# Performance work log

Hardware: AMD Instinct MI355X
Metric: run time of the kernel (lower is better)

Reference implementation:

```python
import jax, jax.numpy as jnp
import numpy as np

B, C, H, W = 2, 256, 64, 64
NUM_HEADS = 4
DIM_HEAD_QK = 64
DIM_HEAD_V = 64  # dim_out // num_heads
DIM_OUT_QK = NUM_HEADS * DIM_HEAD_QK  # 256
DIM_OUT_V = NUM_HEADS * DIM_HEAD_V    # 256
SCALE = DIM_HEAD_QK ** -0.5


def rel_logits_1d(q, rel_k, permute):
    # q: (Bh, Hq, Wq, d), rel_k: (2*Wq-1, d)
    Bh, Hq, Wq, d = q.shape
    R = 2 * Wq - 1
    x = jnp.einsum('bhwd,rd->bhwr', q, rel_k)              # (Bh, Hq, Wq, R)
    x = x.reshape(-1, Wq, R)
    x_pad = jnp.pad(x, ((0, 0), (0, 0), (0, 1))).reshape(x.shape[0], -1)
    x_pad = jnp.pad(x_pad, ((0, 0), (0, Wq - 1)))
    x_pad = x_pad.reshape(-1, Wq + 1, R)
    x = x_pad[:, :Wq, Wq - 1:]                              # (Bh*Hq, Wq, Wq)
    x = x.reshape(Bh, Hq, 1, Wq, Wq)
    x = jnp.broadcast_to(x, (Bh, Hq, Hq, Wq, Wq))
    return jnp.transpose(x, permute)


def pos_embed_rel(q, height_rel, width_rel):
    # q: (Bh, HW, d)
    Bh = q.shape[0]
    qr = q.reshape(Bh, H, W, -1)
    rel_w = rel_logits_1d(qr, width_rel, (0, 1, 3, 2, 4))   # (Bh, H, W, H, W)
    qt = jnp.transpose(qr, (0, 2, 1, 3))                    # (Bh, W, H, d)
    rel_h = rel_logits_1d(qt, height_rel, (0, 3, 1, 4, 2))  # (Bh, H, W, H, W)
    return (rel_h + rel_w).reshape(Bh, H * W, H * W)


def setup_inputs() -> dict:
    key = jax.random.key(0)
    k1, k2, k3, k4 = jax.random.split(key, 4)
    x = jax.random.normal(k1, (B, C, H, W), dtype=jnp.float32)
    qkv_w = jax.random.normal(k2, (2 * DIM_OUT_QK + DIM_OUT_V, C), dtype=jnp.float32) * (C ** -0.5)
    height_rel = jax.random.normal(k3, (2 * H - 1, DIM_HEAD_QK), dtype=jnp.float32) * SCALE
    width_rel = jax.random.normal(k4, (2 * W - 1, DIM_HEAD_QK), dtype=jnp.float32) * SCALE
    return {"x": x, "qkv_w": qkv_w, "height_rel": height_rel, "width_rel": width_rel}


def reference(x, qkv_w, height_rel, width_rel):
    # 1x1 conv == channel matmul
    qkv = jnp.einsum('bchw,oc->bohw', x, qkv_w)             # (B, 768, H, W)
    q, k, v = jnp.split(qkv, [DIM_OUT_QK, 2 * DIM_OUT_QK], axis=1)
    HW = H * W
    q = q.reshape(B * NUM_HEADS, DIM_HEAD_QK, HW).transpose(0, 2, 1)  # (Bh, HW, d)
    k = k.reshape(B * NUM_HEADS, DIM_HEAD_QK, HW)                     # (Bh, d, HW)
    v = v.reshape(B * NUM_HEADS, DIM_HEAD_V, HW).transpose(0, 2, 1)   # (Bh, HW, dv)
    attn = jnp.einsum('bnd,bdm->bnm', q, k) * SCALE + pos_embed_rel(q, height_rel, width_rel)
    attn = jax.nn.softmax(attn, axis=-1)
    out = jnp.einsum('bnm,bmd->bnd', attn, v)               # (Bh, HW, dv)
    out = out.transpose(0, 2, 1).reshape(B, DIM_OUT_V, H, W)
    return out
```

## Files before the change

kernel.cpp:

```cpp
#include <hip/hip_runtime.h>
#include <hip/hip_bf16.h>

typedef __attribute__((ext_vector_type(8))) short bf16x8;
typedef __attribute__((ext_vector_type(4))) float f32x4;

static __device__ __forceinline__ f32x4 mfma16(bf16x8 a, bf16x8 b, f32x4 c) {
    return __builtin_amdgcn_mfma_f32_16x16x32_bf16(a, b, c, 0, 0, 0);
}
static __device__ __forceinline__ void gll16(const void* g, void* l) {
    __builtin_amdgcn_global_load_lds(
        (const __attribute__((address_space(1))) unsigned int*)g,
        (__attribute__((address_space(3))) unsigned int*)l, 16, 0, 0);
}

#define LOG2E 1.44269504f

__global__ __launch_bounds__(256, 4) void qkv_kernel(
    const float* __restrict__ x, const float* __restrict__ w,
    __hip_bfloat16* __restrict__ qb, __hip_bfloat16* __restrict__ kb,
    __hip_bfloat16* __restrict__ vt)
{
    alignas(16) __shared__ __hip_bfloat16 sA[64 * 72];
    alignas(16) __shared__ __hip_bfloat16 sB[64 * 72];
    const int nb = blockIdx.x * 64;
    const int ob = blockIdx.y * 64;
    const int b  = blockIdx.z;
    const int tid  = threadIdx.x;
    const int lane = tid & 63;
    const int wv   = tid >> 6;
    const int quad = lane >> 4;
    const int l16  = lane & 15;

    f32x4 acc[4];
    for (int i = 0; i < 4; i++) acc[i] = (f32x4)0.f;

    for (int k0 = 0; k0 < 256; k0 += 64) {
        __syncthreads();
        {
            const int o = tid >> 2, c0 = (tid & 3) << 4;
            const float* srcw = w + (ob + o) * 256 + k0 + c0;
            union { bf16x8 v; __hip_bfloat16 h[8]; } u0, u1;
            #pragma unroll
            for (int i = 0; i < 2; i++) {
                float4 f = *(const float4*)(srcw + i * 4);
                u0.h[4*i+0] = __float2bfloat16(f.x); u0.h[4*i+1] = __float2bfloat16(f.y);
                u0.h[4*i+2] = __float2bfloat16(f.z); u0.h[4*i+3] = __float2bfloat16(f.w);
            }
            #pragma unroll
            for (int i = 0; i < 2; i++) {
                float4 f = *(const float4*)(srcw + 8 + i * 4);
                u1.h[4*i+0] = __float2bfloat16(f.x); u1.h[4*i+1] = __float2bfloat16(f.y);
                u1.h[4*i+2] = __float2bfloat16(f.z); u1.h[4*i+3] = __float2bfloat16(f.w);
            }
            *(bf16x8*)&sA[o * 72 + c0]     = u0.v;
            *(bf16x8*)&sA[o * 72 + c0 + 8] = u1.v;
        }
        {
            const int c = tid >> 2, n0 = (tid & 3) << 4;
            const int csw = c ^ ((tid & 3) * 16);
            const float* srcx = x + ((size_t)b * 256 + k0 + c) * 4096 + nb + n0;
            #pragma unroll
            for (int i = 0; i < 4; i++) {
                float4 f = *(const float4*)(srcx + i * 4);
                sB[(n0 + 4*i + 0) * 72 + csw] = __float2bfloat16(f.x);
                sB[(n0 + 4*i + 1) * 72 + csw] = __float2bfloat16(f.y);
                sB[(n0 + 4*i + 2) * 72 + csw] = __float2bfloat16(f.z);
                sB[(n0 + 4*i + 3) * 72 + csw] = __float2bfloat16(f.w);
            }
        }
        __syncthreads();
        const __hip_bfloat16* aRow = &sA[(16 * wv + l16) * 72];
        #pragma unroll
        for (int ks = 0; ks < 2; ks++) {
            bf16x8 af = *(const bf16x8*)&aRow[ks * 32 + quad * 8];
            #pragma unroll
            for (int ct = 0; ct < 4; ct++) {
                bf16x8 bfv = *(const bf16x8*)&sB[(16 * ct + l16) * 72
                                                 + ((ks * 32 + quad * 8) ^ (ct * 16))];
                acc[ct] = mfma16(af, bfv, acc[ct]);
            }
        }
    }
    if (ob < 512) {
        #pragma unroll
        for (int ct = 0; ct < 4; ct++) {
            int n = nb + 16 * ct + l16;
            int o0 = ob + 16 * wv + quad * 4;
            union { short4 s; __hip_bfloat16 hh[4]; } u;
            #pragma unroll
            for (int r = 0; r < 4; r++) u.hh[r] = __float2bfloat16(acc[ct][r]);
            int oo = o0 & 255;
            int bhh = b * 4 + (oo >> 6), d = oo & 63;
            if (o0 < 256) {
                *(short4*)(qb + ((size_t)bhh * 4096 + n) * 64 + d) = u.s;
            } else {
                *(short4*)(kb + ((size_t)bhh * 4096 + n) * 64 + (d ^ ((n & 7) << 3))) = u.s;
            }
        }
    } else {
        __syncthreads();
        #pragma unroll
        for (int ct = 0; ct < 4; ct++)
            #pragma unroll
            for (int r = 0; r < 4; r++)
                sA[(16 * wv + quad * 4 + r) * 72 + 16 * ct + l16] = __float2bfloat16(acc[ct][r]);
        int o2 = (ob - 512) + 16 * wv + l16;
        int bhh = b * 4 + (o2 >> 6), d = o2 & 63;
        const __hip_bfloat16* srcl = &sA[(16 * wv + l16) * 72 + 16 * quad];
        __hip_bfloat16* vrow = vt + ((size_t)bhh * 64 + d) * 4096;
        const int kt = quad & 1;
        const int gbase = nb + (quad >> 1) * 32;
        const int dsw = (d & 7) << 3;
        #pragma unroll
        for (int m = 0; m < 4; m++) {
            short4 val = *(const short4*)(srcl + 4 * m);
            int P4 = gbase + 8 * m + 4 * kt;
            *(short4*)(vrow + (P4 ^ dsw)) = val;
        }
    }
}

__global__ __launch_bounds__(512, 4) void attn_kernel(
    const __hip_bfloat16* __restrict__ qb, const __hip_bfloat16* __restrict__ kb,
    const __hip_bfloat16* __restrict__ vt, const float* __restrict__ hrel,
    const float* __restrict__ wrel, float* __restrict__ out)
{
    extern __shared__ __align__(16) char smem[];
    alignas(16) __shared__ __hip_bfloat16 sRH[64 * 66];

    const int h    = blockIdx.x;
    const int bh   = blockIdx.y;
    const int tid  = threadIdx.x;
    const int lane = tid & 63;
    const int wv   = tid >> 6;
    const int qg   = wv >> 2;
    const int kg   = wv & 3;
    const int quad = lane >> 4;
    const int l16  = lane & 15;

    __hip_bfloat16* sQ   = (__hip_bfloat16*)smem;
    __hip_bfloat16* sW   = (__hip_bfloat16*)smem + 64 * 72;
    __hip_bfloat16* sHRs = (__hip_bfloat16*)smem + 192 * 72;
    __hip_bfloat16* sRWt = (__hip_bfloat16*)smem;

    {
        int r = tid >> 3, d8 = (tid & 7) * 8;
        *(bf16x8*)&sQ[r * 72 + d8] =
            *(const bf16x8*)&qb[(((size_t)bh * 4096 + h * 64 + r)) * 64 + d8];
    }
    {
        int r = tid >> 2, c0 = (tid & 3) << 4;
        union { bf16x8 v; __hip_bfloat16 h8[8]; } u0, u1;
        #pragma unroll
        for (int i = 0; i < 2; i++) {
            float4 f = (r < 127) ? *(const float4*)&wrel[r * 64 + c0 + 4*i] : float4{0,0,0,0};
            u0.h8[4*i+0] = __float2bfloat16(f.x); u0.h8[4*i+1] = __float2bfloat16(f.y);
            u0.h8[4*i+2] = __float2bfloat16(f.z); u0.h8[4*i+3] = __float2bfloat16(f.w);
        }
        #pragma unroll
        for (int i = 0; i < 2; i++) {
            float4 f = (r < 127) ? *(const float4*)&wrel[r * 64 + c0 + 8 + 4*i] : float4{0,0,0,0};
            u1.h8[4*i+0] = __float2bfloat16(f.x); u1.h8[4*i+1] = __float2bfloat16(f.y);
            u1.h8[4*i+2] = __float2bfloat16(f.z); u1.h8[4*i+3] = __float2bfloat16(f.w);
        }
        *(bf16x8*)&sW[r * 72 + c0]     = u0.v;
        *(bf16x8*)&sW[r * 72 + c0 + 8] = u1.v;
    }
    {
        int r = tid >> 3, c0 = (tid & 7) * 8;
        union { bf16x8 v; __hip_bfloat16 h8[8]; } u0;
        #pragma unroll
        for (int i = 0; i < 2; i++) {
            float4 f = *(const float4*)&hrel[(63 - h + r) * 64 + c0 + 4*i];
            u0.h8[4*i+0] = __float2bfloat16(f.x); u0.h8[4*i+1] = __float2bfloat16(f.y);
            u0.h8[4*i+2] = __float2bfloat16(f.z); u0.h8[4*i+3] = __float2bfloat16(f.w);
        }
        *(bf16x8*)&sHRs[r * 72 + c0] = u0.v;
    }
    __syncthreads();

    const int g    = wv & 3;
    const int half = wv >> 2;
    const __hip_bfloat16* aRow = &sQ[(16 * g + l16) * 72];
    bf16x8 qf0 = *(const bf16x8*)&aRow[quad * 8];
    bf16x8 qf1 = *(const bf16x8*)&aRow[32 + quad * 8];
    bf16x8 qm[2][2];
    #pragma unroll
    for (int qt = 0; qt < 2; qt++) {
        const __hip_bfloat16* qr = &sQ[(qg * 32 + 16 * qt + l16) * 72];
        qm[qt][0] = *(const bf16x8*)&qr[quad * 8];
        qm[qt][1] = *(const bf16x8*)&qr[32 + quad * 8];
    }
    __syncthreads();

    {
        const int rbase = half * 64;
        #pragma unroll
        for (int ct = 0; ct < 4; ct++) {
            int rr = rbase + 16 * ct + l16;
            f32x4 a = (f32x4)0.f;
            a = mfma16(qf0, *(const bf16x8*)&sW[rr * 72 + quad * 8], a);
            a = mfma16(qf1, *(const bf16x8*)&sW[rr * 72 + 32 + quad * 8], a);
            #pragma unroll
            for (int r = 0; r < 4; r++) {
                int ww = 16 * g + quad * 4 + r;
                int wp = rr + ww - 63;
                if (wp >= 0 && wp < 64) sRWt[ww * 68 + wp] = __float2bfloat16(a[r]);
            }
        }
    }
    if (half == 0) {
        #pragma unroll
        for (int ct = 0; ct < 4; ct++) {
            f32x4 a = (f32x4)0.f;
            a = mfma16(qf0, *(const bf16x8*)&sHRs[(16 * ct + l16) * 72 + quad * 8], a);
            a = mfma16(qf1, *(const bf16x8*)&sHRs[(16 * ct + l16) * 72 + 32 + quad * 8], a);
            #pragma unroll
            for (int r = 0; r < 4; r++)
                sRH[(16 * g + quad * 4 + r) * 66 + 16 * ct + l16] = __float2bfloat16(a[r]);
        }
    }
    __syncthreads();

    union S4 { short4 s; __hip_bfloat16 h[4]; };
    S4 rwp[2][2];
    #pragma unroll
    for (int qt = 0; qt < 2; qt++)
        #pragma unroll
        for (int kt = 0; kt < 2; kt++)
            rwp[qt][kt].s = *(const short4*)&sRWt[(qg * 32 + 16 * qt + l16) * 68
                                                  + 32 * (kg & 1) + 16 * kt + 4 * quad];
    __syncthreads();

    const char* kT = (const char*)kb + (size_t)bh * 524288 + wv * 1024 + lane * 16;
    const char* vT = (const char*)vt + (size_t)bh * 524288
                     + (size_t)(wv * 4 + quad) * 8192 + l16 * 16;

    gll16(kT,           smem + wv * 1024);
    gll16(kT + 8192,    smem + 8192 + wv * 1024);
    gll16(vT,           smem + 16384 + wv * 1024);
    gll16(vT + 262144,  smem + 24576 + wv * 1024);
    __syncthreads();

    f32x4 oacc[2][4];
    #pragma unroll
    for (int qt = 0; qt < 2; qt++)
        #pragma unroll
        for (int dt = 0; dt < 4; dt++) oacc[qt][dt] = (f32x4)0.f;
    float lsum[2] = {0.f, 0.f};

    const int krowOff = (kg * 32 + l16) * 128;
    const int sw  = (l16 & 7) << 4;
    const int kA  = (quad * 16) ^ sw;
    const int kB  = (64 + quad * 16) ^ sw;
    const int vOff = 16384 + l16 * 256 + ((kg * 64 + quad * 16) ^ sw);

    const __hip_bfloat16* rh0 = &sRH[(qg * 32 + l16) * 66];
    const __hip_bfloat16* rh1 = &sRH[(qg * 32 + 16 + l16) * 66];

    for (int j = 0; j < 32; j++) {
        const char* buf = smem + (j & 1) * 32768;
        if (j < 31) {
            char* nbuf = smem + ((j + 1) & 1) * 32768;
            const char* gk = kT + (size_t)(j + 1) * 16384;
            gll16(gk,          nbuf + wv * 1024);
            gll16(gk + 8192,   nbuf + 8192 + wv * 1024);
            const char* gv = vT + (size_t)(j + 1) * 256;
            gll16(gv,          nbuf + 16384 + wv * 1024);
            gll16(gv + 262144, nbuf + 24576 + wv * 1024);
        }

        const char* kr = buf + krowOff;
        bf16x8 kf00 = *(const bf16x8*)(kr + kA);
        bf16x8 kf01 = *(const bf16x8*)(kr + kB);
        bf16x8 kf10 = *(const bf16x8*)(kr + 2048 + kA);
        bf16x8 kf11 = *(const bf16x8*)(kr + 2048 + kB);

        const int hp = 2 * j + (kg >> 1);
        bf16x8 pa[2];
        #pragma unroll
        for (int qt = 0; qt < 2; qt++) {
            f32x4 s0 = (f32x4)0.f, s1 = (f32x4)0.f;
            s0 = mfma16(kf00, qm[qt][0], s0);
            s0 = mfma16(kf01, qm[qt][1], s0);
            s1 = mfma16(kf10, qm[qt][0], s1);
            s1 = mfma16(kf11, qm[qt][1], s1);
            float rhb = LOG2E * __bfloat162float((qt ? rh1 : rh0)[hp]);
            union { bf16x8 v; __hip_bfloat16 hh[8]; } pu;
            #pragma unroll
            for (int r = 0; r < 4; r++) {
                float p = __builtin_amdgcn_exp2f(
                    fmaf(s0[r], 0.125f * LOG2E,
                         fmaf(__bfloat162float(rwp[qt][0].h[r]), LOG2E, rhb)));
                lsum[qt] += p;
                pu.hh[r] = __float2bfloat16(p);
            }
            #pragma unroll
            for (int r = 0; r < 4; r++) {
                float p = __builtin_amdgcn_exp2f(
                    fmaf(s1[r], 0.125f * LOG2E,
                         fmaf(__bfloat162float(rwp[qt][1].h[r]), LOG2E, rhb)));
                lsum[qt] += p;
                pu.hh[4 + r] = __float2bfloat16(p);
            }
            pa[qt] = pu.v;
        }

        #pragma unroll
        for (int dt = 0; dt < 4; dt++) {
            bf16x8 vf = *(const bf16x8*)(buf + vOff + dt * 4096);
            oacc[0][dt] = mfma16(pa[0], vf, oacc[0][dt]);
            oacc[1][dt] = mfma16(pa[1], vf, oacc[1][dt]);
        }
        __syncthreads();
    }

    #pragma unroll
    for (int qt = 0; qt < 2; qt++) {
        lsum[qt] += __shfl_xor(lsum[qt], 16, 64);
        lsum[qt] += __shfl_xor(lsum[qt], 32, 64);
    }

    float* obuf  = (float*)smem;
    float* slbuf = obuf + 4608;
    for (int rnd = 1; rnd < 4; rnd++) {
        if (kg == rnd) {
            #pragma unroll
            for (int qt = 0; qt < 2; qt++)
                #pragma unroll
                for (int dt = 0; dt < 4; dt++)
                    *(f32x4*)&obuf[qg * 2304 + (16 * dt + l16) * 36 + 16 * qt + 4 * quad]
                        = oacc[qt][dt];
            if (quad == 0) {
                slbuf[qg * 64 + l16]      = lsum[0];
                slbuf[qg * 64 + 16 + l16] = lsum[1];
            }
        }
        __syncthreads();
        if (kg == 0) {
            #pragma unroll
            for (int qt = 0; qt < 2; qt++)
                #pragma unroll
                for (int dt = 0; dt < 4; dt++)
                    oacc[qt][dt] += *(const f32x4*)&obuf[qg * 2304 + (16 * dt + l16) * 36
                                                          + 16 * qt + 4 * quad];
            lsum[0] += slbuf[qg * 64 + l16];
            lsum[1] += slbuf[qg * 64 + 16 + l16];
        }
        __syncthreads();
    }

    if (kg == 0) {
        if (quad == 0) {
            slbuf[qg * 64 + l16]      = lsum[0];
            slbuf[qg * 64 + 16 + l16] = lsum[1];
        }
        const int b = bh >> 2, head = bh & 3;
        #pragma unroll
        for (int qt = 0; qt < 2; qt++) {
            f32x4 lv;
            #pragma unroll
            for (int r = 0; r < 4; r++)
                lv[r] = 1.f / slbuf[qg * 64 + 16 * qt + 4 * quad + r];
            #pragma unroll
            for (int dt = 0; dt < 4; dt++) {
                f32x4 o = oacc[qt][dt] * lv;
                int dv = 16 * dt + l16;
                int q0 = qg * 32 + 16 * qt + 4 * quad;
                *(f32x4*)&out[((size_t)(b * 256 + head * 64 + dv)) * 4096 + h * 64 + q0] = o;
            }
        }
    }
}

extern "C" void kernel_launch(void* const* d_in, const int* in_sizes, int n_in,
                              void* d_out, int out_size, void* d_ws, size_t ws_size,
                              hipStream_t stream) {
    const float* x     = (const float*)d_in[0];
    const float* qkv_w = (const float*)d_in[1];
    const float* hrel  = (const float*)d_in[2];
    const float* wrel  = (const float*)d_in[3];
    float* out = (float*)d_out;

    __hip_bfloat16* qb = (__hip_bfloat16*)d_ws;
    __hip_bfloat16* kb = qb + (size_t)8 * 4096 * 64;
    __hip_bfloat16* vt = kb + (size_t)8 * 4096 * 64;

    qkv_kernel<<<dim3(64, 12, 2), 256, 0, stream>>>(x, qkv_w, qb, kb, vt);
    attn_kernel<<<dim3(64, 8), 512, 65536, stream>>>(qb, kb, vt, hrel, wrel, out);
}
```

Before: 131.5 us.

## Compute softmax row sums via MFMA, stage QK stores through LDS, single-pass reduction

Several changes land together. The QKV kernel now stages Q/K tiles through shared memory so each thread writes two 16-byte vectors instead of scattered 8-byte stores. The attention loop precomputes LOG2E-scaled relative-width biases, uses paired bf16 conversion, and replaces per-lane scalar row-sum accumulation with an extra MFMA against a ones vector. It also adds s_setprio around the MFMA phases and collapses the three-round cross-warp reduction into one write and one read phase. The extra MFMAs and larger LDS reduction buffers are the trade-off for fewer VALU ops and fewer barriers.

```diff
diff --git a/kernel.cpp b/kernel.cpp
--- a/kernel.cpp
+++ b/kernel.cpp
@@ -82,20 +82,30 @@
         }
     }
     if (ob < 512) {
+        __syncthreads();
         #pragma unroll
         for (int ct = 0; ct < 4; ct++) {
-            int n = nb + 16 * ct + l16;
-            int o0 = ob + 16 * wv + quad * 4;
             union { short4 s; __hip_bfloat16 hh[4]; } u;
             #pragma unroll
             for (int r = 0; r < 4; r++) u.hh[r] = __float2bfloat16(acc[ct][r]);
-            int oo = o0 & 255;
-            int bhh = b * 4 + (oo >> 6), d = oo & 63;
-            if (o0 < 256) {
-                *(short4*)(qb + ((size_t)bhh * 4096 + n) * 64 + d) = u.s;
-            } else {
-                *(short4*)(kb + ((size_t)bhh * 4096 + n) * 64 + (d ^ ((n & 7) << 3))) = u.s;
-            }
+            *(short4*)&sA[(16 * ct + l16) * 72 + 16 * wv + 4 * quad] = u.s;
+        }
+        __syncthreads();
+        const int n_l = tid >> 2, d16 = (tid & 3) * 16;
+        const int n = nb + n_l;
+        const __hip_bfloat16* srcl = &sA[n_l * 72 + d16];
+        bf16x8 v0 = *(const bf16x8*)srcl;
+        bf16x8 v1 = *(const bf16x8*)(srcl + 8);
+        const int bhh = b * 4 + ((ob & 255) >> 6);
+        if (ob < 256) {
+            __hip_bfloat16* dst = qb + ((size_t)bhh * 4096 + n) * 64;
+            *(bf16x8*)(dst + d16)     = v0;
+            *(bf16x8*)(dst + d16 + 8) = v1;
+        } else {
+            const int s = (n & 7) << 3;
+            __hip_bfloat16* dst = kb + ((size_t)bhh * 4096 + n) * 64;
+            *(bf16x8*)(dst + (d16 ^ s))       = v0;
+            *(bf16x8*)(dst + ((d16 + 8) ^ s)) = v1;
         }
     } else {
         __syncthreads();
@@ -223,13 +233,18 @@
     __syncthreads();
 
     union S4 { short4 s; __hip_bfloat16 h[4]; };
-    S4 rwp[2][2];
+    float rwf[2][2][4];
     #pragma unroll
     for (int qt = 0; qt < 2; qt++)
         #pragma unroll
-        for (int kt = 0; kt < 2; kt++)
-            rwp[qt][kt].s = *(const short4*)&sRWt[(qg * 32 + 16 * qt + l16) * 68
-                                                  + 32 * (kg & 1) + 16 * kt + 4 * quad];
+        for (int kt = 0; kt < 2; kt++) {
+            S4 t;
+            t.s = *(const short4*)&sRWt[(qg * 32 + 16 * qt + l16) * 68
+                                        + 32 * (kg & 1) + 16 * kt + 4 * quad];
+            #pragma unroll
+            for (int r = 0; r < 4; r++)
+                rwf[qt][kt][r] = LOG2E * __bfloat162float(t.h[r]);
+        }
     __syncthreads();
 
     const char* kT = (const char*)kb + (size_t)bh * 524288 + wv * 1024 + lane * 16;
@@ -247,7 +262,8 @@
     for (int qt = 0; qt < 2; qt++)
         #pragma unroll
         for (int dt = 0; dt < 4; dt++) oacc[qt][dt] = (f32x4)0.f;
-    float lsum[2] = {0.f, 0.f};
+    f32x4 lacc[2] = {(f32x4)0.f, (f32x4)0.f};
+    const bf16x8 vones = (bf16x8)(short)0x3F80;
 
     const int krowOff = (kg * 32 + l16) * 128;
     const int sw  = (l16 & 7) << 4;
@@ -257,6 +273,7 @@
 
     const __hip_bfloat16* rh0 = &sRH[(qg * 32 + l16) * 66];
     const __hip_bfloat16* rh1 = &sRH[(qg * 32 + 16 + l16) * 66];
+    const float SC = 0.125f * LOG2E;
 
     for (int j = 0; j < 32; j++) {
         const char* buf = smem + (j & 1) * 32768;
@@ -276,92 +293,89 @@
         bf16x8 kf10 = *(const bf16x8*)(kr + 2048 + kA);
         bf16x8 kf11 = *(const bf16x8*)(kr + 2048 + kB);
 
+        f32x4 s[2][2];
+        __builtin_amdgcn_s_setprio(1);
+        #pragma unroll
+        for (int qt = 0; qt < 2; qt++) {
+            f32x4 a0 = (f32x4)0.f, a1 = (f32x4)0.f;
+            a0 = mfma16(kf00, qm[qt][0], a0);
+            a0 = mfma16(kf01, qm[qt][1], a0);
+            a1 = mfma16(kf10, qm[qt][0], a1);
+            a1 = mfma16(kf11, qm[qt][1], a1);
+            s[qt][0] = a0; s[qt][1] = a1;
+        }
+        __builtin_amdgcn_s_setprio(0);
+
         const int hp = 2 * j + (kg >> 1);
         bf16x8 pa[2];
         #pragma unroll
         for (int qt = 0; qt < 2; qt++) {
-            f32x4 s0 = (f32x4)0.f, s1 = (f32x4)0.f;
-            s0 = mfma16(kf00, qm[qt][0], s0);
-            s0 = mfma16(kf01, qm[qt][1], s0);
-            s1 = mfma16(kf10, qm[qt][0], s1);
-            s1 = mfma16(kf11, qm[qt][1], s1);
             float rhb = LOG2E * __bfloat162float((qt ? rh1 : rh0)[hp]);
-            union { bf16x8 v; __hip_bfloat16 hh[8]; } pu;
-            #pragma unroll
-            for (int r = 0; r < 4; r++) {
-                float p = __builtin_amdgcn_exp2f(
-                    fmaf(s0[r], 0.125f * LOG2E,
-                         fmaf(__bfloat162float(rwp[qt][0].h[r]), LOG2E, rhb)));
-                lsum[qt] += p;
-                pu.hh[r] = __float2bfloat16(p);
-            }
-            #pragma unroll
-            for (int r = 0; r < 4; r++) {
-                float p = __builtin_amdgcn_exp2f(
-                    fmaf(s1[r], 0.125f * LOG2E,
-                         fmaf(__bfloat162float(rwp[qt][1].h[r]), LOG2E, rhb)));
-                lsum[qt] += p;
-                pu.hh[4 + r] = __float2bfloat16(p);
-            }
+            float pv[8];
+            #pragma unroll
+            for (int r = 0; r < 4; r++)
+                pv[r] = __builtin_amdgcn_exp2f(fmaf(s[qt][0][r], SC, rwf[qt][0][r] + rhb));
+            #pragma unroll
+            for (int r = 0; r < 4; r++)
+                pv[4 + r] = __builtin_amdgcn_exp2f(fmaf(s[qt][1][r], SC, rwf[qt][1][r] + rhb));
+            union { bf16x8 v; __hip_bfloat162 b2[4]; } pu;
+            #pragma unroll
+            for (int pi = 0; pi < 4; pi++)
+                pu.b2[pi] = __float22bfloat162_rn(float2{pv[2 * pi], pv[2 * pi + 1]});
             pa[qt] = pu.v;
         }
 
+        __builtin_amdgcn_s_setprio(1);
         #pragma unroll
         for (int dt = 0; dt < 4; dt++) {
             bf16x8 vf = *(const bf16x8*)(buf + vOff + dt * 4096);
             oacc[0][dt] = mfma16(pa[0], vf, oacc[0][dt]);
             oacc[1][dt] = mfma16(pa[1], vf, oacc[1][dt]);
         }
-        __syncthreads();
-    }
-
-    #pragma unroll
-    for (int qt = 0; qt < 2; qt++) {
-        lsum[qt] += __shfl_xor(lsum[qt], 16, 64);
-        lsum[qt] += __shfl_xor(lsum[qt], 32, 64);
-    }
-
-    float* obuf  = (float*)smem;
-    float* slbuf = obuf + 4608;
-    for (int rnd = 1; rnd < 4; rnd++) {
-        if (kg == rnd) {
+        lacc[0] = mfma16(pa[0], vones, lacc[0]);
+        lacc[1] = mfma16(pa[1], vones, lacc[1]);
+        __builtin_amdgcn_s_setprio(0);
+        __syncthreads();
+    }
+
+    float* obuf = (float*)smem;
+    if (kg != 0) {
+        float* rb = obuf + (kg - 1) * 4672;
+        #pragma unroll
+        for (int qt = 0; qt < 2; qt++)
+            #pragma unroll
+            for (int dt = 0; dt < 4; dt++)
+                *(f32x4*)&rb[qg * 2304 + (16 * dt + l16) * 36 + 16 * qt + 4 * quad]
+                    = oacc[qt][dt];
+        if (l16 == 0)
             #pragma unroll
             for (int qt = 0; qt < 2; qt++)
                 #pragma unroll
-                for (int dt = 0; dt < 4; dt++)
-                    *(f32x4*)&obuf[qg * 2304 + (16 * dt + l16) * 36 + 16 * qt + 4 * quad]
-                        = oacc[qt][dt];
-            if (quad == 0) {
-                slbuf[qg * 64 + l16]      = lsum[0];
-                slbuf[qg * 64 + 16 + l16] = lsum[1];
-            }
-        }
-        __syncthreads();
-        if (kg == 0) {
-            #pragma unroll
-            for (int qt = 0; qt < 2; qt++)
+                for (int r = 0; r < 4; r++)
+                    rb[4608 + qg * 32 + 16 * qt + 4 * quad + r] = lacc[qt][r];
+    }
+    __syncthreads();
+    if (kg == 0) {
+        #pragma unroll
+        for (int rg = 0; rg < 3; rg++) {
+            const float* rb = obuf + rg * 4672;
+            #pragma unroll
+            for (int qt = 0; qt < 2; qt++) {
                 #pragma unroll
                 for (int dt = 0; dt < 4; dt++)
-                    oacc[qt][dt] += *(const f32x4*)&obuf[qg * 2304 + (16 * dt + l16) * 36
-                                                          + 16 * qt + 4 * quad];
-            lsum[0] += slbuf[qg * 64 + l16];
-            lsum[1] += slbuf[qg * 64 + 16 + l16];
-        }
-        __syncthreads();
-    }
-
-    if (kg == 0) {
-        if (quad == 0) {
-            slbuf[qg * 64 + l16]      = lsum[0];
-            slbuf[qg * 64 + 16 + l16] = lsum[1];
+                    oacc[qt][dt] += *(const f32x4*)&rb[qg * 2304 + (16 * dt + l16) * 36
+                                                       + 16 * qt + 4 * quad];
+                #pragma unroll
+                for (int r = 0; r < 4; r++)
+                    lacc[qt][r] += rb[4608 + qg * 32 + 16 * qt + 4 * quad + r];
+            }
         }
         const int b = bh >> 2, head = bh & 3;
         #pragma unroll
         for (int qt = 0; qt < 2; qt++) {
             f32x4 lv;
             #pragma unroll
-            for (int r = 0; r < 4; r++)
-                lv[r] = 1.f / slbuf[qg * 64 + 16 * qt + 4 * quad + r];
+            for (int r = 0; r < 4; r++) lv[r] = 1.f / lacc[qt][r];
             #pragma unroll
             for (int dt = 0; dt < 4; dt++) {
                 f32x4 o = oacc[qt][dt] * lv;
```

Result: faster. 125.4 us (-4.7%).
